# Performance work log

Measured on AMD Instinct MI355X. Metric: run time of the kernel, lower is better.

Reference implementation:

```python
import jax, jax.numpy as jnp
import numpy as np

DIM = 1024
HEADS = 16
HEAD_DIM = DIM // HEADS
EPS = 1e-6

def _layernorm(x, gamma, beta):
    # LayerNorm over last axis (head_dim), biased variance like torch
    mu = jnp.mean(x, axis=-1, keepdims=True)
    var = jnp.mean(jnp.square(x - mu), axis=-1, keepdims=True)
    return (x - mu) * jax.lax.rsqrt(var + EPS) * gamma + beta

def setup_inputs() -> dict:
    key = jax.random.key(0)
    ks = jax.random.split(key, 12)
    B, N, D = 2, 2048, DIM
    s = 1.0 / np.sqrt(D)
    inp = {
        'x': jax.random.normal(ks[0], (B, N, D), jnp.float32),
        'attn_bias': jax.random.normal(ks[1], (B, 1, N, N), jnp.float32),
        'Wq': jax.random.normal(ks[2], (D, D), jnp.float32) * s,
        'bq': jnp.zeros((D,), jnp.float32),
        'Wk': jax.random.normal(ks[3], (D, D), jnp.float32) * s,
        'bk': jnp.zeros((D,), jnp.float32),
        'Wv': jax.random.normal(ks[4], (D, D), jnp.float32) * s,
        'bv': jnp.zeros((D,), jnp.float32),
        'Wo': jax.random.normal(ks[5], (D, D), jnp.float32) * s,
        'bo': jnp.zeros((D,), jnp.float32),
        'q_gamma': jnp.ones((HEAD_DIM,), jnp.float32),
        'q_beta': jnp.zeros((HEAD_DIM,), jnp.float32),
        'k_gamma': jnp.ones((HEAD_DIM,), jnp.float32),
        'k_beta': jnp.zeros((HEAD_DIM,), jnp.float32),
    }
    return inp

def reference(x, attn_bias, Wq, bq, Wk, bk, Wv, bv, Wo, bo, q_gamma, q_beta, k_gamma, k_beta):
    B, N, D = x.shape
    h, dh = HEADS, HEAD_DIM
    # QKV projections (torch Linear: x @ W.T + b) -> (B, h, N, dh)
    def proj(W, b):
        y = jnp.einsum('bnd,ed->bne', x, W) + b
        return y.reshape(B, N, h, dh).transpose(0, 2, 1, 3)
    q = proj(Wq, bq)
    k = proj(Wk, bk)
    v = proj(Wv, bv)
    # per-head LayerNorm on Q and K
    q = _layernorm(q, q_gamma, q_beta)
    k = _layernorm(k, k_gamma, k_beta)
    # scaled dot-product attention with additive graph bias
    scores = jnp.einsum('bhnd,bhmd->bhnm', q, k) / np.sqrt(dh).astype(np.float32)
    scores = scores + attn_bias  # (B,1,N,N) broadcasts over heads
    attn = jax.nn.softmax(scores, axis=-1)
    out = jnp.einsum('bhnm,bhmd->bhnd', attn, v)
    out = out.transpose(0, 2, 1, 3).reshape(B, N, D)
    return jnp.einsum('bnd,ed->bne', out, Wo) + bo
```

## Files before the change

kernel.cpp:

```cpp
#include <hip/hip_runtime.h>
#include <hip/hip_bf16.h>

#define D_MODEL 1024
#define N_SEQ   2048
#define N_B     2
#define M_ROWS  (N_B * N_SEQ)

typedef __attribute__((ext_vector_type(8))) short bf16x8;
typedef __attribute__((ext_vector_type(4))) float f32x4;

typedef const __attribute__((address_space(1))) unsigned int gu32_t;
typedef __attribute__((address_space(3))) unsigned int lu32_t;

__device__ __forceinline__ void gload16(const void* g, void* l) {
  __builtin_amdgcn_global_load_lds((gu32_t*)g, (lu32_t*)l, 16, 0, 0);
}

__device__ inline unsigned short f2bf(float f) {
  union { float f; unsigned int u; } v; v.f = f;
  unsigned int r = (v.u + 0x7FFFu + ((v.u >> 16) & 1u)) >> 16;
  return (unsigned short)r;
}

__device__ __forceinline__ unsigned int cvt_pk_bf16(float a, float b) {
  unsigned int r;
  asm("v_cvt_pk_bf16_f32 %0, %1, %2" : "=v"(r) : "v"(a), "v"(b));
  return r;
}

__device__ __forceinline__ float exp2fast(float x) {
#if __has_builtin(__builtin_amdgcn_exp2f)
  return __builtin_amdgcn_exp2f(x);
#else
  return __expf(x * 0.69314718056f);
#endif
}

__device__ __forceinline__ int lds_off(int row, int col ) {
  return row * 64 + (((col >> 3) ^ (row & 7)) << 3) + (col & 7);
}

template<int ROWS>
__device__ __forceinline__ void stage_tile(const unsigned short* gbase, size_t gstride,
                                           unsigned short* lds, int tid) {
  const int wave = tid >> 6;
#pragma unroll
  for (int rnd = 0; rnd < ROWS / 32; ++rnd) {
    int c = rnd * 256 + tid;
    int row = c >> 3, pc = c & 7;
    int gcol = ((pc ^ (row & 7)) << 3);
    gload16(gbase + (size_t)row * gstride + gcol,
            lds + (size_t)(rnd * 256 + wave * 64) * 8);
  }
}

constexpr size_t XEL = (size_t)M_ROWS * D_MODEL;
constexpr size_t WEL = (size_t)D_MODEL * D_MODEL;

__launch_bounds__(256)
__global__ void cvt_kernel(const float* __restrict__ x,
                           const float* __restrict__ wq, const float* __restrict__ wk,
                           const float* __restrict__ wv, const float* __restrict__ wo,
                           unsigned short* __restrict__ dst) {
  size_t i = ((size_t)blockIdx.x * 256 + threadIdx.x) * 8;
  if (i >= XEL + 4 * WEL) return;
  const float* s; size_t off = i;
  if (off < XEL)                { s = x; }
  else if (off < XEL + WEL)     { s = wq; off -= XEL; }
  else if (off < XEL + 2*WEL)   { s = wk; off -= XEL + WEL; }
  else if (off < XEL + 3*WEL)   { s = wv; off -= XEL + 2*WEL; }
  else                          { s = wo; off -= XEL + 3*WEL; }
  float4 f0 = *(const float4*)(s + off);
  float4 f1 = *(const float4*)(s + off + 4);
  unsigned short t[8] = { f2bf(f0.x), f2bf(f0.y), f2bf(f0.z), f2bf(f0.w),
                          f2bf(f1.x), f2bf(f1.y), f2bf(f1.z), f2bf(f1.w) };
  *(uint4*)(dst + i) = *(const uint4*)t;
}

__device__ __forceinline__ void mainloop128(const unsigned short* __restrict__ A,
                                            const unsigned short* __restrict__ Bw,
                                            int m0, int e0,
                                            unsigned short* As, unsigned short* Bs,
                                            f32x4 (&acc)[4][4]) {
  const int tid  = threadIdx.x;
  const int wave = tid >> 6, lane = tid & 63;
  const int l16 = lane & 15, quad = lane >> 4;
  const int wr = wave >> 1, wc = wave & 1;

  for (int kt = 0; kt < D_MODEL / 64; ++kt) {
    const int k0 = kt * 64;
    stage_tile<128>(A + (size_t)m0 * D_MODEL + k0, D_MODEL, As, tid);
    stage_tile<128>(Bw + (size_t)e0 * D_MODEL + k0, D_MODEL, Bs, tid);
    __syncthreads();
#pragma unroll
    for (int ks = 0; ks < 2; ++ks) {
      bf16x8 af[4], bfr[4];
#pragma unroll
      for (int mi = 0; mi < 4; ++mi)
        af[mi] = *(const bf16x8*)(As + lds_off(wr * 64 + mi * 16 + l16, ks * 32 + quad * 8));
#pragma unroll
      for (int ci = 0; ci < 4; ++ci)
        bfr[ci] = *(const bf16x8*)(Bs + lds_off(wc * 64 + ci * 16 + l16, ks * 32 + quad * 8));
#pragma unroll
      for (int mi = 0; mi < 4; ++mi)
#pragma unroll
        for (int ci = 0; ci < 4; ++ci)
          acc[mi][ci] = __builtin_amdgcn_mfma_f32_16x16x32_bf16(af[mi], bfr[ci], acc[mi][ci], 0, 0, 0);
    }
    __syncthreads();
  }
}

__launch_bounds__(256)
__global__ void qkv_gemm(const unsigned short* __restrict__ xb,
                         const unsigned short* __restrict__ wb,
                         const float* __restrict__ bq, const float* __restrict__ bk,
                         const float* __restrict__ bv,
                         const float* __restrict__ qg, const float* __restrict__ qbeta,
                         const float* __restrict__ kg, const float* __restrict__ kbeta,
                         unsigned short* __restrict__ qkout,
                         unsigned short* __restrict__ vt) {
  __shared__ unsigned short As[128 * 64];
  __shared__ unsigned short Bs[128 * 64];
  const int m0  = blockIdx.x * 128;
  const int by  = blockIdx.y;
  const int mat = by >> 3;
  const int e0  = (by & 7) * 128;
  const unsigned short* Bw = wb + (size_t)mat * WEL;

  f32x4 acc[4][4];
#pragma unroll
  for (int mi = 0; mi < 4; ++mi)
#pragma unroll
    for (int ci = 0; ci < 4; ++ci) acc[mi][ci] = f32x4{0.f, 0.f, 0.f, 0.f};

  mainloop128(xb, Bw, m0, e0, As, Bs, acc);

  const int lane = threadIdx.x & 63, wave = threadIdx.x >> 6;
  const int l16 = lane & 15, quad = lane >> 4;
  const int wr = wave >> 1, wc = wave & 1;
  const int colbase = e0 + wc * 64;

  const float* bias = (mat == 0) ? bq : ((mat == 1) ? bk : bv);
  float bcol[4];
#pragma unroll
  for (int ci = 0; ci < 4; ++ci) bcol[ci] = bias[colbase + ci * 16 + l16];
#pragma unroll
  for (int mi = 0; mi < 4; ++mi)
#pragma unroll
    for (int ci = 0; ci < 4; ++ci)
#pragma unroll
      for (int r = 0; r < 4; ++r) acc[mi][ci][r] += bcol[ci];

  if (mat < 2) {
    const float* gamma = (mat == 0) ? qg : kg;
    const float* beta  = (mat == 0) ? qbeta : kbeta;
    const float sc = (mat == 0) ? 0.18033688011112042f : 1.0f;
    float g4[4], bt4[4];
#pragma unroll
    for (int ci = 0; ci < 4; ++ci) {
      g4[ci] = gamma[ci * 16 + l16] * sc;
      bt4[ci] = beta[ci * 16 + l16] * sc;
    }
#pragma unroll
    for (int mi = 0; mi < 4; ++mi)
#pragma unroll
      for (int r = 0; r < 4; ++r) {
        float s = acc[mi][0][r] + acc[mi][1][r] + acc[mi][2][r] + acc[mi][3][r];
        s += __shfl_xor(s, 1); s += __shfl_xor(s, 2);
        s += __shfl_xor(s, 4); s += __shfl_xor(s, 8);
        float mean = s * (1.f / 64.f);
        float d0 = acc[mi][0][r] - mean, d1 = acc[mi][1][r] - mean;
        float d2 = acc[mi][2][r] - mean, d3 = acc[mi][3][r] - mean;
        float q = d0 * d0 + d1 * d1 + d2 * d2 + d3 * d3;
        q += __shfl_xor(q, 1); q += __shfl_xor(q, 2);
        q += __shfl_xor(q, 4); q += __shfl_xor(q, 8);
        float rs = rsqrtf(q * (1.f / 64.f) + 1e-6f);
        acc[mi][0][r] = d0 * rs * g4[0] + bt4[0];
        acc[mi][1][r] = d1 * rs * g4[1] + bt4[1];
        acc[mi][2][r] = d2 * rs * g4[2] + bt4[2];
        acc[mi][3][r] = d3 * rs * g4[3] + bt4[3];
      }
    unsigned short* out = qkout + (size_t)mat * XEL;
#pragma unroll
    for (int mi = 0; mi < 4; ++mi)
#pragma unroll
      for (int ci = 0; ci < 4; ++ci) {
        int col = colbase + ci * 16 + l16;
#pragma unroll
        for (int r = 0; r < 4; ++r) {
          int row = m0 + wr * 64 + mi * 16 + quad * 4 + r;
          out[(size_t)row * D_MODEL + col] = f2bf(acc[mi][ci][r]);
        }
      }
  } else {
    unsigned short* scr = ((wave < 2) ? As : Bs) + (size_t)(wave & 1) * 4096;
#pragma unroll
    for (int ci = 0; ci < 4; ++ci) {
      int dl = ci * 16 + l16;
      int sw = (dl & 3) * 16;
#pragma unroll
      for (int mi = 0; mi < 4; ++mi)
#pragma unroll
        for (int r = 0; r < 4; ++r) {
          int np = ((mi >> 1) << 5) + (quad << 3) + ((mi & 1) << 2) + r;
          scr[dl * 64 + (np ^ sw)] = f2bf(acc[mi][ci][r]);
        }
    }
    __builtin_amdgcn_wave_barrier();
    int row0 = m0 + wr * 64;
    int b = row0 >> 11, nb = row0 & 2047;
    int h = colbase >> 6;
    int dl = lane;
    unsigned short* gdst = vt + ((size_t)((b * 16 + h) * 64 + dl) * N_SEQ + nb);
    const unsigned short* srow = scr + dl * 64;
    int sw = (dl & 3) * 16;
#pragma unroll
    for (int j = 0; j < 8; ++j) {
      uint4 vv = *(const uint4*)(srow + ((j * 8) ^ sw));
      *(uint4*)(gdst + j * 8) = vv;
    }
  }
}

__launch_bounds__(256)
__global__ void out_gemm(const unsigned short* __restrict__ ao,
                         const unsigned short* __restrict__ wob,
                         const float* __restrict__ bo,
                         float* __restrict__ out) {
  __shared__ unsigned short As[128 * 64];
  __shared__ unsigned short Bs[128 * 64];
  const int m0 = blockIdx.x * 128;
  const int e0 = blockIdx.y * 128;

  f32x4 acc[4][4];
#pragma unroll
  for (int mi = 0; mi < 4; ++mi)
#pragma unroll
    for (int ci = 0; ci < 4; ++ci) acc[mi][ci] = f32x4{0.f, 0.f, 0.f, 0.f};

  mainloop128(ao, wob, m0, e0, As, Bs, acc);

  const int lane = threadIdx.x & 63, wave = threadIdx.x >> 6;
  const int l16 = lane & 15, quad = lane >> 4;
  const int wr = wave >> 1, wc = wave & 1;
  float bcol[4];
#pragma unroll
  for (int ci = 0; ci < 4; ++ci) bcol[ci] = bo[e0 + wc * 64 + ci * 16 + l16];
#pragma unroll
  for (int mi = 0; mi < 4; ++mi)
#pragma unroll
    for (int ci = 0; ci < 4; ++ci) {
      int col = e0 + wc * 64 + ci * 16 + l16;
#pragma unroll
      for (int r = 0; r < 4; ++r) {
        int row = m0 + wr * 64 + mi * 16 + quad * 4 + r;
        out[(size_t)row * D_MODEL + col] = acc[mi][ci][r] + bcol[ci];
      }
    }
}

__launch_bounds__(256)
__global__ void attn_kernel(const unsigned short* __restrict__ Q,
                            const unsigned short* __restrict__ Kn,
                            const unsigned short* __restrict__ Vt,
                            const float* __restrict__ bias,
                            unsigned short* __restrict__ Out) {
  __shared__ unsigned short Qs[128 * 64];
  __shared__ unsigned short Ks[2][64 * 64];
  __shared__ unsigned short Vts[2][64 * 64];
  const int tid  = threadIdx.x;
  const int wave = tid >> 6, lane = tid & 63;
  const int quad = lane >> 4, l16 = lane & 15;
  const int bidx = blockIdx.x;
  const int qt = bidx & 15;
  const int h  = (bidx >> 4) & 15;
  const int b  = bidx >> 8;
  const int q0 = qt * 128;
  const size_t base  = (size_t)b * N_SEQ * D_MODEL + (size_t)h * 64;
  const unsigned short* vtb = Vt + (size_t)(b * 16 + h) * 64 * N_SEQ;

  stage_tile<128>(Q + base + (size_t)q0 * D_MODEL, D_MODEL, Qs, tid);
  stage_tile<64>(Kn + base, D_MODEL, Ks[0], tid);
  stage_tile<64>(vtb, N_SEQ, Vts[0], tid);

  const float* brow[2];
#pragma unroll
  for (int mi = 0; mi < 2; ++mi)
    brow[mi] = bias + ((size_t)b * N_SEQ + q0 + wave * 32 + mi * 16 + l16) * N_SEQ;

  f32x4 bcur[2][4], bnxt[2][4];
#pragma unroll
  for (int mi = 0; mi < 2; ++mi)
#pragma unroll
    for (int c = 0; c < 4; ++c)
      bcur[mi][c] = *(const f32x4*)(brow[mi] + c * 16 + quad * 4);

  __syncthreads();
  bf16x8 aq[2][2];
#pragma unroll
  for (int mi = 0; mi < 2; ++mi)
#pragma unroll
    for (int ks = 0; ks < 2; ++ks)
      aq[mi][ks] = *(const bf16x8*)(Qs + lds_off(wave * 32 + mi * 16 + l16, ks * 32 + quad * 8));

  f32x4 o[2][4];
#pragma unroll
  for (int mi = 0; mi < 2; ++mi)
#pragma unroll
    for (int cd = 0; cd < 4; ++cd) o[mi][cd] = f32x4{0.f, 0.f, 0.f, 0.f};
  float lsum[2] = {0.f, 0.f};
  constexpr float LOG2E = 1.44269504088896340736f;

  constexpr int NT = N_SEQ / 64;
  for (int kt = 0; kt < NT; ++kt) {
    const int cur = kt & 1;
    if (kt + 1 < NT) {
      stage_tile<64>(Kn + base + (size_t)(kt + 1) * 64 * D_MODEL, D_MODEL, Ks[cur ^ 1], tid);
      stage_tile<64>(vtb + (kt + 1) * 64, N_SEQ, Vts[cur ^ 1], tid);
#pragma unroll
      for (int mi = 0; mi < 2; ++mi)
#pragma unroll
        for (int c = 0; c < 4; ++c)
          bnxt[mi][c] = *(const f32x4*)(brow[mi] + (kt + 1) * 64 + c * 16 + quad * 4);
    }

    f32x4 sfT[2][4];
#pragma unroll
    for (int c = 0; c < 4; ++c) {
      bf16x8 k0 = *(const bf16x8*)(Ks[cur] + lds_off(c * 16 + l16, quad * 8));
      bf16x8 k1 = *(const bf16x8*)(Ks[cur] + lds_off(c * 16 + l16, 32 + quad * 8));
#pragma unroll
      for (int mi = 0; mi < 2; ++mi) {
        f32x4 z = f32x4{0.f, 0.f, 0.f, 0.f};
        z = __builtin_amdgcn_mfma_f32_16x16x32_bf16(k0, aq[mi][0], z, 0, 0, 0);
        sfT[mi][c] = __builtin_amdgcn_mfma_f32_16x16x32_bf16(k1, aq[mi][1], z, 0, 0, 0);
      }
    }

    union PafU { unsigned int w[4]; bf16x8 v; };
    PafU paf[2][2];
#pragma unroll
    for (int mi = 0; mi < 2; ++mi)
#pragma unroll
      for (int c = 0; c < 4; ++c) {
        float p0 = exp2fast(fmaf(bcur[mi][c][0], LOG2E, sfT[mi][c][0]));
        float p1 = exp2fast(fmaf(bcur[mi][c][1], LOG2E, sfT[mi][c][1]));
        float p2 = exp2fast(fmaf(bcur[mi][c][2], LOG2E, sfT[mi][c][2]));
        float p3 = exp2fast(fmaf(bcur[mi][c][3], LOG2E, sfT[mi][c][3]));
        lsum[mi] += (p0 + p1) + (p2 + p3);
        paf[mi][c >> 1].w[(c & 1) * 2]     = cvt_pk_bf16(p0, p1);
        paf[mi][c >> 1].w[(c & 1) * 2 + 1] = cvt_pk_bf16(p2, p3);
      }

#pragma unroll
    for (int ks = 0; ks < 2; ++ks) {
      bf16x8 bv[4];
#pragma unroll
      for (int cd = 0; cd < 4; ++cd)
        bv[cd] = *(const bf16x8*)(Vts[cur] + lds_off(cd * 16 + l16, ks * 32 + quad * 8));
#pragma unroll
      for (int mi = 0; mi < 2; ++mi)
#pragma unroll
        for (int cd = 0; cd < 4; ++cd)
          o[mi][cd] = __builtin_amdgcn_mfma_f32_16x16x32_bf16(bv[cd], paf[mi][ks].v, o[mi][cd], 0, 0, 0);
    }
    __syncthreads();
#pragma unroll
    for (int mi = 0; mi < 2; ++mi)
#pragma unroll
      for (int c = 0; c < 4; ++c) bcur[mi][c] = bnxt[mi][c];
  }

#pragma unroll
  for (int mi = 0; mi < 2; ++mi) {
    float l = lsum[mi];
    l += __shfl_xor(l, 16);
    l += __shfl_xor(l, 32);
    float inv = 1.0f / l;
    size_t row = (size_t)b * N_SEQ + q0 + wave * 32 + mi * 16 + l16;
#pragma unroll
    for (int cd = 0; cd < 4; ++cd) {
      uint2 vv;
      vv.x = cvt_pk_bf16(o[mi][cd][0] * inv, o[mi][cd][1] * inv);
      vv.y = cvt_pk_bf16(o[mi][cd][2] * inv, o[mi][cd][3] * inv);
      *(uint2*)(Out + row * D_MODEL + h * 64 + cd * 16 + quad * 4) = vv;
    }
  }
}

extern "C" void kernel_launch(void* const* d_in, const int* in_sizes, int n_in,
                              void* d_out, int out_size, void* d_ws, size_t ws_size,
                              hipStream_t stream) {
  const float* x    = (const float*)d_in[0];
  const float* bias = (const float*)d_in[1];
  const float* Wq = (const float*)d_in[2];  const float* bq = (const float*)d_in[3];
  const float* Wk = (const float*)d_in[4];  const float* bk = (const float*)d_in[5];
  const float* Wv = (const float*)d_in[6];  const float* bv = (const float*)d_in[7];
  const float* Wo = (const float*)d_in[8];  const float* bo = (const float*)d_in[9];
  const float* qg = (const float*)d_in[10]; const float* qb = (const float*)d_in[11];
  const float* kg = (const float*)d_in[12]; const float* kb = (const float*)d_in[13];
  float* out = (float*)d_out;

  unsigned short* wsb = (unsigned short*)d_ws;
  unsigned short* xb  = wsb;
  unsigned short* wqb = wsb + XEL;
  unsigned short* wob = wsb + XEL + 3 * WEL;
  unsigned short* qn  = wsb + XEL + 4 * WEL;
  unsigned short* kn  = qn + XEL;
  unsigned short* vt  = qn + 2 * XEL;
  unsigned short* ao  = xb;

  dim3 blk(256, 1, 1);

  cvt_kernel<<<dim3((unsigned)((XEL + 4 * WEL) / (256 * 8)), 1, 1), blk, 0, stream>>>(
      x, Wq, Wk, Wv, Wo, wsb);

  qkv_gemm<<<dim3(M_ROWS / 128, 24, 1), blk, 0, stream>>>(
      xb, wqb, bq, bk, bv, qg, qb, kg, kb, qn, vt);

  attn_kernel<<<dim3(N_B * 16 * (N_SEQ / 128), 1, 1), blk, 0, stream>>>(qn, kn, vt, bias, ao);

  out_gemm<<<dim3(M_ROWS / 128, D_MODEL / 128, 1), blk, 0, stream>>>(ao, wob, bo, out);
}
```

Before: 263.3 us.

## Split attention key tiles across wave pairs with LDS reduction

The attention kernel now runs 512 threads per block, and each pair of waves shares a 32-row query slice. Each wave in a pair handles half of every 64-key tile, covering both the scores and the PV accumulation. The partial outputs and row sums are combined through LDS at the end. This doubles the waves available to hide latency and halves per-wave register state, at the cost of a final LDS reduction and more threads contending at the per-tile barrier.

```diff
diff --git a/kernel.cpp b/kernel.cpp
--- a/kernel.cpp
+++ b/kernel.cpp
@@ -40,17 +40,17 @@
   return row * 64 + (((col >> 3) ^ (row & 7)) << 3) + (col & 7);
 }
 
-template<int ROWS>
+template<int ROWS, int NTHR = 256>
 __device__ __forceinline__ void stage_tile(const unsigned short* gbase, size_t gstride,
                                            unsigned short* lds, int tid) {
   const int wave = tid >> 6;
 #pragma unroll
-  for (int rnd = 0; rnd < ROWS / 32; ++rnd) {
-    int c = rnd * 256 + tid;
+  for (int rnd = 0; rnd < ROWS * 8 / NTHR; ++rnd) {
+    int c = rnd * NTHR + tid;
     int row = c >> 3, pc = c & 7;
     int gcol = ((pc ^ (row & 7)) << 3);
     gload16(gbase + (size_t)row * gstride + gcol,
-            lds + (size_t)(rnd * 256 + wave * 64) * 8);
+            lds + (size_t)(rnd * NTHR + wave * 64) * 8);
   }
 }
 
@@ -260,18 +260,20 @@
     }
 }
 
-__launch_bounds__(256)
+__launch_bounds__(512)
 __global__ void attn_kernel(const unsigned short* __restrict__ Q,
                             const unsigned short* __restrict__ Kn,
                             const unsigned short* __restrict__ Vt,
                             const float* __restrict__ bias,
                             unsigned short* __restrict__ Out) {
-  __shared__ unsigned short Qs[128 * 64];
-  __shared__ unsigned short Ks[2][64 * 64];
-  __shared__ unsigned short Vts[2][64 * 64];
+  __shared__ unsigned short smem[24576];
+  unsigned short* Qs = smem;
+
   const int tid  = threadIdx.x;
   const int wave = tid >> 6, lane = tid & 63;
   const int quad = lane >> 4, l16 = lane & 15;
+  const int pairId = wave >> 1;
+  const int kh = wave & 1;
   const int bidx = blockIdx.x;
   const int qt = bidx & 15;
   const int h  = (bidx >> 4) & 15;
@@ -280,21 +282,22 @@
   const size_t base  = (size_t)b * N_SEQ * D_MODEL + (size_t)h * 64;
   const unsigned short* vtb = Vt + (size_t)(b * 16 + h) * 64 * N_SEQ;
 
-  stage_tile<128>(Q + base + (size_t)q0 * D_MODEL, D_MODEL, Qs, tid);
-  stage_tile<64>(Kn + base, D_MODEL, Ks[0], tid);
-  stage_tile<64>(vtb, N_SEQ, Vts[0], tid);
+  stage_tile<128, 512>(Q + base + (size_t)q0 * D_MODEL, D_MODEL, Qs, tid);
+  stage_tile<64, 512>(Kn + base, D_MODEL, smem + 8192, tid);
+  stage_tile<64, 512>(vtb, N_SEQ, smem + 16384, tid);
 
   const float* brow[2];
 #pragma unroll
   for (int mi = 0; mi < 2; ++mi)
-    brow[mi] = bias + ((size_t)b * N_SEQ + q0 + wave * 32 + mi * 16 + l16) * N_SEQ;
-
-  f32x4 bcur[2][4], bnxt[2][4];
+    brow[mi] = bias + ((size_t)b * N_SEQ + q0 + pairId * 32 + mi * 16 + l16) * N_SEQ;
+  const int bcol0 = kh * 32 + quad * 4;
+
+  f32x4 bcur[2][2], bnxt[2][2];
 #pragma unroll
   for (int mi = 0; mi < 2; ++mi)
 #pragma unroll
-    for (int c = 0; c < 4; ++c)
-      bcur[mi][c] = *(const f32x4*)(brow[mi] + c * 16 + quad * 4);
+    for (int cl = 0; cl < 2; ++cl)
+      bcur[mi][cl] = *(const f32x4*)(brow[mi] + bcol0 + cl * 16);
 
   __syncthreads();
   bf16x8 aq[2][2];
@@ -302,7 +305,7 @@
   for (int mi = 0; mi < 2; ++mi)
 #pragma unroll
     for (int ks = 0; ks < 2; ++ks)
-      aq[mi][ks] = *(const bf16x8*)(Qs + lds_off(wave * 32 + mi * 16 + l16, ks * 32 + quad * 8));
+      aq[mi][ks] = *(const bf16x8*)(Qs + lds_off(pairId * 32 + mi * 16 + l16, ks * 32 + quad * 8));
 
   f32x4 o[2][4];
 #pragma unroll
@@ -315,76 +318,106 @@
   constexpr int NT = N_SEQ / 64;
   for (int kt = 0; kt < NT; ++kt) {
     const int cur = kt & 1;
+    unsigned short* Kcur = smem + 8192 + cur * 4096;
+    unsigned short* Vcur = smem + 16384 + cur * 4096;
     if (kt + 1 < NT) {
-      stage_tile<64>(Kn + base + (size_t)(kt + 1) * 64 * D_MODEL, D_MODEL, Ks[cur ^ 1], tid);
-      stage_tile<64>(vtb + (kt + 1) * 64, N_SEQ, Vts[cur ^ 1], tid);
+      stage_tile<64, 512>(Kn + base + (size_t)(kt + 1) * 64 * D_MODEL, D_MODEL,
+                          smem + 8192 + (cur ^ 1) * 4096, tid);
+      stage_tile<64, 512>(vtb + (kt + 1) * 64, N_SEQ,
+                          smem + 16384 + (cur ^ 1) * 4096, tid);
 #pragma unroll
       for (int mi = 0; mi < 2; ++mi)
 #pragma unroll
-        for (int c = 0; c < 4; ++c)
-          bnxt[mi][c] = *(const f32x4*)(brow[mi] + (kt + 1) * 64 + c * 16 + quad * 4);
-    }
-
-    f32x4 sfT[2][4];
-#pragma unroll
-    for (int c = 0; c < 4; ++c) {
-      bf16x8 k0 = *(const bf16x8*)(Ks[cur] + lds_off(c * 16 + l16, quad * 8));
-      bf16x8 k1 = *(const bf16x8*)(Ks[cur] + lds_off(c * 16 + l16, 32 + quad * 8));
+        for (int cl = 0; cl < 2; ++cl)
+          bnxt[mi][cl] = *(const f32x4*)(brow[mi] + (kt + 1) * 64 + bcol0 + cl * 16);
+    }
+
+    f32x4 sfT[2][2];
+#pragma unroll
+    for (int cl = 0; cl < 2; ++cl) {
+      const int c = kh * 2 + cl;
+      bf16x8 k0 = *(const bf16x8*)(Kcur + lds_off(c * 16 + l16, quad * 8));
+      bf16x8 k1 = *(const bf16x8*)(Kcur + lds_off(c * 16 + l16, 32 + quad * 8));
 #pragma unroll
       for (int mi = 0; mi < 2; ++mi) {
         f32x4 z = f32x4{0.f, 0.f, 0.f, 0.f};
         z = __builtin_amdgcn_mfma_f32_16x16x32_bf16(k0, aq[mi][0], z, 0, 0, 0);
-        sfT[mi][c] = __builtin_amdgcn_mfma_f32_16x16x32_bf16(k1, aq[mi][1], z, 0, 0, 0);
+        sfT[mi][cl] = __builtin_amdgcn_mfma_f32_16x16x32_bf16(k1, aq[mi][1], z, 0, 0, 0);
       }
     }
 
     union PafU { unsigned int w[4]; bf16x8 v; };
-    PafU paf[2][2];
+    PafU paf[2];
 #pragma unroll
     for (int mi = 0; mi < 2; ++mi)
 #pragma unroll
-      for (int c = 0; c < 4; ++c) {
-        float p0 = exp2fast(fmaf(bcur[mi][c][0], LOG2E, sfT[mi][c][0]));
-        float p1 = exp2fast(fmaf(bcur[mi][c][1], LOG2E, sfT[mi][c][1]));
-        float p2 = exp2fast(fmaf(bcur[mi][c][2], LOG2E, sfT[mi][c][2]));
-        float p3 = exp2fast(fmaf(bcur[mi][c][3], LOG2E, sfT[mi][c][3]));
+      for (int cl = 0; cl < 2; ++cl) {
+        float p0 = exp2fast(fmaf(bcur[mi][cl][0], LOG2E, sfT[mi][cl][0]));
+        float p1 = exp2fast(fmaf(bcur[mi][cl][1], LOG2E, sfT[mi][cl][1]));
+        float p2 = exp2fast(fmaf(bcur[mi][cl][2], LOG2E, sfT[mi][cl][2]));
+        float p3 = exp2fast(fmaf(bcur[mi][cl][3], LOG2E, sfT[mi][cl][3]));
         lsum[mi] += (p0 + p1) + (p2 + p3);
-        paf[mi][c >> 1].w[(c & 1) * 2]     = cvt_pk_bf16(p0, p1);
-        paf[mi][c >> 1].w[(c & 1) * 2 + 1] = cvt_pk_bf16(p2, p3);
-      }
-
-#pragma unroll
-    for (int ks = 0; ks < 2; ++ks) {
+        paf[mi].w[cl * 2]     = cvt_pk_bf16(p0, p1);
+        paf[mi].w[cl * 2 + 1] = cvt_pk_bf16(p2, p3);
+      }
+
+    {
       bf16x8 bv[4];
 #pragma unroll
       for (int cd = 0; cd < 4; ++cd)
-        bv[cd] = *(const bf16x8*)(Vts[cur] + lds_off(cd * 16 + l16, ks * 32 + quad * 8));
+        bv[cd] = *(const bf16x8*)(Vcur + lds_off(cd * 16 + l16, kh * 32 + quad * 8));
 #pragma unroll
       for (int mi = 0; mi < 2; ++mi)
 #pragma unroll
         for (int cd = 0; cd < 4; ++cd)
-          o[mi][cd] = __builtin_amdgcn_mfma_f32_16x16x32_bf16(bv[cd], paf[mi][ks].v, o[mi][cd], 0, 0, 0);
+          o[mi][cd] = __builtin_amdgcn_mfma_f32_16x16x32_bf16(bv[cd], paf[mi].v, o[mi][cd], 0, 0, 0);
     }
     __syncthreads();
 #pragma unroll
     for (int mi = 0; mi < 2; ++mi)
 #pragma unroll
-      for (int c = 0; c < 4; ++c) bcur[mi][c] = bnxt[mi][c];
-  }
-
-#pragma unroll
-  for (int mi = 0; mi < 2; ++mi) {
-    float l = lsum[mi];
-    l += __shfl_xor(l, 16);
-    l += __shfl_xor(l, 32);
-    float inv = 1.0f / l;
-    size_t row = (size_t)b * N_SEQ + q0 + wave * 32 + mi * 16 + l16;
-#pragma unroll
-    for (int cd = 0; cd < 4; ++cd) {
-      uint2 vv;
-      vv.x = cvt_pk_bf16(o[mi][cd][0] * inv, o[mi][cd][1] * inv);
-      vv.y = cvt_pk_bf16(o[mi][cd][2] * inv, o[mi][cd][3] * inv);
-      *(uint2*)(Out + row * D_MODEL + h * 64 + cd * 16 + quad * 4) = vv;
+      for (int cl = 0; cl < 2; ++cl) bcur[mi][cl] = bnxt[mi][cl];
+  }
+
+  float* red = (float*)smem;
+  float* slot = red + (size_t)(pairId * 64 + lane) * 34;
+  if (kh) {
+#pragma unroll
+    for (int mi = 0; mi < 2; ++mi)
+#pragma unroll
+      for (int cd = 0; cd < 4; ++cd)
+#pragma unroll
+        for (int r = 0; r < 4; ++r)
+          slot[mi * 16 + cd * 4 + r] = o[mi][cd][r];
+    slot[32] = lsum[0];
+    slot[33] = lsum[1];
+  }
+  __syncthreads();
+  if (!kh) {
+#pragma unroll
+    for (int mi = 0; mi < 2; ++mi)
+#pragma unroll
+      for (int cd = 0; cd < 4; ++cd)
+#pragma unroll
+        for (int r = 0; r < 4; ++r)
+          o[mi][cd][r] += slot[mi * 16 + cd * 4 + r];
+    lsum[0] += slot[32];
+    lsum[1] += slot[33];
+
+#pragma unroll
+    for (int mi = 0; mi < 2; ++mi) {
+      float l = lsum[mi];
+      l += __shfl_xor(l, 16);
+      l += __shfl_xor(l, 32);
+      float inv = 1.0f / l;
+      size_t row = (size_t)b * N_SEQ + q0 + pairId * 32 + mi * 16 + l16;
+#pragma unroll
+      for (int cd = 0; cd < 4; ++cd) {
+        uint2 vv;
+        vv.x = cvt_pk_bf16(o[mi][cd][0] * inv, o[mi][cd][1] * inv);
+        vv.y = cvt_pk_bf16(o[mi][cd][2] * inv, o[mi][cd][3] * inv);
+        *(uint2*)(Out + row * D_MODEL + h * 64 + cd * 16 + quad * 4) = vv;
+      }
     }
   }
 }
@@ -419,7 +452,8 @@
   qkv_gemm<<<dim3(M_ROWS / 128, 24, 1), blk, 0, stream>>>(
       xb, wqb, bq, bk, bv, qg, qb, kg, kb, qn, vt);
 
-  attn_kernel<<<dim3(N_B * 16 * (N_SEQ / 128), 1, 1), blk, 0, stream>>>(qn, kn, vt, bias, ao);
+  attn_kernel<<<dim3(N_B * 16 * (N_SEQ / 128), 1, 1), dim3(512, 1, 1), 0, stream>>>(
+      qn, kn, vt, bias, ao);
 
   out_gemm<<<dim3(M_ROWS / 128, D_MODEL / 128, 1), blk, 0, stream>>>(ao, wob, bo, out);
 }
```

New measurement: 259.1 us. About the same (-1.6%).
